# Performance work log

Measured on AMD Instinct MI355X. Metric: run time of the kernel, lower is better.

## Reference

```python
import jax, jax.numpy as jnp
import numpy as np

B, N, DIM = 4, 8192, 1024
HEADS, DIM_HEAD = 16, 64


def setup_inputs() -> dict:
    key = jax.random.key(0)
    ks = jax.random.split(key, 6)
    s = 1.0 / np.sqrt(DIM_HEAD)
    so = 1.0 / np.sqrt(HEADS * DIM_HEAD)
    return {
        "x": jax.random.normal(ks[0], (B, N, DIM), dtype=jnp.float32),
        "Wq": jax.random.uniform(ks[1], (DIM_HEAD, DIM_HEAD), jnp.float32, -s, s),
        "Wk": jax.random.uniform(ks[2], (DIM_HEAD, DIM_HEAD), jnp.float32, -s, s),
        "Wv": jax.random.uniform(ks[3], (DIM_HEAD, DIM_HEAD), jnp.float32, -s, s),
        "Wo": jax.random.uniform(ks[4], (DIM, HEADS * DIM_HEAD), jnp.float32, -so, so),
        "bo": jax.random.uniform(ks[5], (DIM,), jnp.float32, -so, so),
    }


def reference(x, Wq, Wk, Wv, Wo, bo):
    Bs, Ns, Cs = x.shape
    # [B, H, N, Dh]
    xh = x.reshape(Bs, Ns, HEADS, DIM_HEAD).transpose(0, 2, 1, 3)
    # torch Linear: y = x @ W.T
    q = jnp.einsum('bhnd,ed->bhne', xh, Wq)
    k = jnp.einsum('bhnd,ed->bhne', xh, Wk)
    v = jnp.einsum('bhnd,ed->bhne', xh, Wv)
    # k^T v: [B, H, Dh, Dh], normalized by N (dropout is identity, p=0)
    dots = jnp.einsum('bhnd,bhne->bhde', k, v) / float(Ns)
    res = jnp.einsum('bhnd,bhde->bhne', q, dots)
    # b h n d -> b n (h d)
    res = res.transpose(0, 2, 1, 3).reshape(Bs, Ns, HEADS * DIM_HEAD)
    return res @ Wo.T + bo
```

## Files before the change

### kernel.cpp

```cpp
#include <hip/hip_runtime.h>

#define DIMC 1024
#define NSEQ 8192
#define DH 64

typedef __attribute__((ext_vector_type(8))) short short8;
typedef __attribute__((ext_vector_type(4))) float f32x4;

__device__ __forceinline__ short f2bf(float f) {
  union { float f; unsigned u; } v; v.f = f;
  unsigned r = v.u + 0x7FFFu + ((v.u >> 16) & 1u);
  return (short)(r >> 16);
}

__device__ __forceinline__ void gload_lds16(const void* g, void* l) {
  __builtin_amdgcn_global_load_lds(
      (const __attribute__((address_space(1))) void*)g,
      (__attribute__((address_space(3))) void*)l, 16, 0, 0);
}

__global__ __launch_bounds__(64) void gram_kernel(const float* __restrict__ x,
                                                  float* __restrict__ Gpart) {
  int chunk = blockIdx.x, bh = blockIdx.y;
  int b = bh >> 4, h = bh & 15;
  int t = threadIdx.x;
  __shared__ __align__(16) float rows[16 * 64];
  const float* xb = x + ((size_t)b * NSEQ) * DIMC + h * DH;
  int d0 = (t >> 3) * 8, e0 = (t & 7) * 8;
  float acc[8][8] = {};
  for (int it = 0; it < 16; it++) {
    int nbase = chunk * 256 + it * 16;
    float4 v[4];
#pragma unroll
    for (int i = 0; i < 4; i++) {
      int f4 = i * 64 + t;
      v[i] = *(const float4*)(xb + (size_t)(nbase + (f4 >> 4)) * DIMC + (f4 & 15) * 4);
    }
    __syncthreads();
#pragma unroll
    for (int i = 0; i < 4; i++) ((float4*)rows)[i * 64 + t] = v[i];
    __syncthreads();
#pragma unroll
    for (int r = 0; r < 16; r++) {
      float xd[8], xe[8];
      *(float4*)&xd[0] = *(const float4*)&rows[r * 64 + d0];
      *(float4*)&xd[4] = *(const float4*)&rows[r * 64 + d0 + 4];
      *(float4*)&xe[0] = *(const float4*)&rows[r * 64 + e0];
      *(float4*)&xe[4] = *(const float4*)&rows[r * 64 + e0 + 4];
#pragma unroll
      for (int i = 0; i < 8; i++)
#pragma unroll
        for (int j = 0; j < 8; j++) acc[i][j] = fmaf(xd[i], xe[j], acc[i][j]);
    }
  }
  float* gp = Gpart + (size_t)chunk * (64 * 4096) + (size_t)bh * 4096;
#pragma unroll
  for (int i = 0; i < 8; i++)
#pragma unroll
    for (int j = 0; j < 8; j++) gp[(d0 + i) * 64 + e0 + j] = acc[i][j];
}

__global__ void reduce_g(const float* __restrict__ Gpart, float* __restrict__ G) {
  int i = blockIdx.x * 256 + threadIdx.x;
  float s = 0.f;
#pragma unroll
  for (int p = 0; p < 32; p++) s += Gpart[(size_t)p * (64 * 4096) + i];
  G[i] = s;
}

__global__ __launch_bounds__(256) void combine_kernel(
    const float* __restrict__ G, const float* __restrict__ Wq,
    const float* __restrict__ Wk, const float* __restrict__ Wv,
    const float* __restrict__ Wo, short* __restrict__ WbigT) {
  int bh = blockIdx.x, qt = blockIdx.y;
  int b = bh >> 4, h = bh & 15;
  int t = threadIdx.x;
  __shared__ __align__(16) float sG[4096];
  __shared__ __align__(16) float sW[4096];
  __shared__ __align__(16) float sA[4096];
  __shared__ __align__(16) float sM[4096];

  for (int i = t; i < 4096; i += 256) sG[i] = G[(size_t)bh * 4096 + i];
  for (int i = t; i < 4096; i += 256) sW[i] = Wk[i];
  __syncthreads();

  int d0 = (t >> 4) * 4, e0 = (t & 15) * 4;
  {
    float a[4][4] = {};
    for (int fg = 0; fg < 16; fg++) {
      float wk[4][4], g4[4][4];
#pragma unroll
      for (int i = 0; i < 4; i++) *(float4*)wk[i] = *(const float4*)&sW[(d0 + i) * 64 + fg * 4];
#pragma unroll
      for (int ff = 0; ff < 4; ff++) *(float4*)g4[ff] = *(const float4*)&sG[(fg * 4 + ff) * 64 + e0];
#pragma unroll
      for (int i = 0; i < 4; i++)
#pragma unroll
        for (int ff = 0; ff < 4; ff++)
#pragma unroll
          for (int j = 0; j < 4; j++) a[i][j] = fmaf(wk[i][ff], g4[ff][j], a[i][j]);
    }
#pragma unroll
    for (int i = 0; i < 4; i++)
#pragma unroll
      for (int j = 0; j < 4; j++) sA[(d0 + i) * 64 + e0 + j] = a[i][j];
  }
  __syncthreads();
  for (int i = t; i < 4096; i += 256) sW[i] = Wv[i];
  __syncthreads();
  {
    float a[4][4] = {};
    for (int fgi = 0; fgi < 16; fgi++) {
      int fg = (fgi + (t & 15)) & 15;
      float t1[4][4], wv[4][4];
#pragma unroll
      for (int i = 0; i < 4; i++) *(float4*)t1[i] = *(const float4*)&sA[(d0 + i) * 64 + fg * 4];
#pragma unroll
      for (int j = 0; j < 4; j++) *(float4*)wv[j] = *(const float4*)&sW[(e0 + j) * 64 + fg * 4];
#pragma unroll
      for (int i = 0; i < 4; i++)
#pragma unroll
        for (int j = 0; j < 4; j++)
#pragma unroll
          for (int ff = 0; ff < 4; ff++) a[i][j] = fmaf(t1[i][ff], wv[j][ff], a[i][j]);
    }
    __syncthreads();
#pragma unroll
    for (int i = 0; i < 4; i++)
#pragma unroll
      for (int j = 0; j < 4; j++) sG[(d0 + i) * 64 + e0 + j] = a[i][j];
  }
  __syncthreads();
  for (int i = t; i < 4096; i += 256) sW[i] = Wq[i];
  __syncthreads();
  {
    float a[4][4] = {};
    for (int f = 0; f < 64; f++) {
      float wq[4], t2[4];
      *(float4*)wq = *(const float4*)&sW[f * 64 + d0];
      *(float4*)t2 = *(const float4*)&sG[f * 64 + e0];
#pragma unroll
      for (int i = 0; i < 4; i++)
#pragma unroll
        for (int j = 0; j < 4; j++) a[i][j] = fmaf(wq[i], t2[j], a[i][j]);
    }
#pragma unroll
    for (int i = 0; i < 4; i++)
#pragma unroll
      for (int j = 0; j < 4; j++) sM[(d0 + i) * 64 + e0 + j] = a[i][j] * (1.0f / 8192.0f);
  }
  __syncthreads();
  int dd0 = (t & 15) * 4, cl0 = (t >> 4) * 4;
  for (int cc = qt * 4; cc < qt * 4 + 4; cc++) {
    int c0 = cc * 64;
    for (int i = t; i < 4096; i += 256)
      sW[i] = Wo[(size_t)(c0 + (i >> 6)) * DIMC + h * DH + (i & 63)];
    __syncthreads();
    float a[4][4] = {};
    for (int egi = 0; egi < 16; egi++) {
      int eg = (egi + (t & 15)) & 15;
      float m4[4][4], wo4[4][4];
#pragma unroll
      for (int i = 0; i < 4; i++) *(float4*)m4[i] = *(const float4*)&sM[(dd0 + i) * 64 + eg * 4];
#pragma unroll
      for (int j = 0; j < 4; j++) *(float4*)wo4[j] = *(const float4*)&sW[(cl0 + j) * 64 + eg * 4];
#pragma unroll
      for (int i = 0; i < 4; i++)
#pragma unroll
        for (int j = 0; j < 4; j++)
#pragma unroll
          for (int ff = 0; ff < 4; ff++) a[i][j] = fmaf(m4[i][ff], wo4[j][ff], a[i][j]);
    }
#pragma unroll
    for (int j = 0; j < 4; j++)
#pragma unroll
      for (int i = 0; i < 4; i++)
        WbigT[((size_t)b << 20) + (size_t)(c0 + cl0 + j) * DIMC + h * DH + dd0 + i] =
            f2bf(a[i][j]);
    __syncthreads();
  }
}

__global__ __launch_bounds__(256, 2) void gemm_kernel(
    const float* __restrict__ x, const short* __restrict__ WbigT,
    const float* __restrict__ bo, float* __restrict__ out) {
  int bid = blockIdx.x;
  int xcd = bid & 7, r = bid >> 3;
  int g = r >> 5, q = r & 31;
  int m_blk = g * 32 + xcd * 4 + (q >> 3);
  int n_blk = q & 7;
  int b = m_blk >> 6;
  int row0 = m_blk * 128;
  int c0 = n_blk * 128;

  __shared__ __align__(16) short As[128 * 32];
  __shared__ __align__(16) short Bs[128 * 32];

  int t = threadIdx.x;
  int lane = t & 63, wave = t >> 6;
  int wm = wave >> 1, wn = wave & 1;
  int quad = lane >> 4, ln = lane & 15;

  f32x4 acc[4][4];
#pragma unroll
  for (int i = 0; i < 4; i++)
#pragma unroll
    for (int j = 0; j < 4; j++) acc[i][j] = (f32x4){0.f, 0.f, 0.f, 0.f};

  const short* Bbase = WbigT + ((size_t)b << 20);

  for (int kt = 0; kt < 32; kt++) {
    int k0 = kt * 32;
    __syncthreads();
#pragma unroll
    for (int L = 0; L < 2; L++) {
      int elem = (wave * 2 + L) * 512 + lane * 8;
      int crow = elem >> 5, koff = elem & 31;
      gload_lds16(Bbase + (size_t)(c0 + crow) * DIMC + k0 + koff, &Bs[elem]);
    }
#pragma unroll
    for (int qq = 0; qq < 2; qq++) {
      int elem = qq * 2048 + wave * 512 + lane * 8;
      int m = elem >> 5, kk = elem & 31;
      const float* gp = x + (size_t)(row0 + m) * DIMC + k0 + kk;
      float4 v0 = *(const float4*)gp;
      float4 v1 = *(const float4*)(gp + 4);
      short8 pk;
      pk[0] = f2bf(v0.x); pk[1] = f2bf(v0.y); pk[2] = f2bf(v0.z); pk[3] = f2bf(v0.w);
      pk[4] = f2bf(v1.x); pk[5] = f2bf(v1.y); pk[6] = f2bf(v1.z); pk[7] = f2bf(v1.w);
      *(short8*)&As[elem] = pk;
    }
    __syncthreads();
    short8 afrag[4], bfrag[4];
#pragma unroll
    for (int i = 0; i < 4; i++) {
      afrag[i] = *(const short8*)&As[(wm * 64 + i * 16 + ln) * 32 + quad * 8];
      bfrag[i] = *(const short8*)&Bs[(wn * 64 + i * 16 + ln) * 32 + quad * 8];
    }
#pragma unroll
    for (int i = 0; i < 4; i++)
#pragma unroll
      for (int j = 0; j < 4; j++)
        acc[i][j] = __builtin_amdgcn_mfma_f32_16x16x32_bf16(afrag[i], bfrag[j], acc[i][j], 0, 0, 0);
  }

  float bov[4];
#pragma unroll
  for (int j = 0; j < 4; j++) bov[j] = bo[c0 + wn * 64 + j * 16 + ln];
#pragma unroll
  for (int i = 0; i < 4; i++)
#pragma unroll
    for (int j = 0; j < 4; j++) {
      int col = c0 + wn * 64 + j * 16 + ln;
#pragma unroll
      for (int rr = 0; rr < 4; rr++) {
        int row = row0 + wm * 64 + i * 16 + quad * 4 + rr;
        out[(size_t)row * DIMC + col] = acc[i][j][rr] + bov[j];
      }
    }
}

extern "C" void kernel_launch(void* const* d_in, const int* in_sizes, int n_in,
                              void* d_out, int out_size, void* d_ws, size_t ws_size,
                              hipStream_t stream) {
  const float* x  = (const float*)d_in[0];
  const float* Wq = (const float*)d_in[1];
  const float* Wk = (const float*)d_in[2];
  const float* Wv = (const float*)d_in[3];
  const float* Wo = (const float*)d_in[4];
  const float* bo = (const float*)d_in[5];
  float* out = (float*)d_out;

  float* Gpart = (float*)d_ws;
  float* G     = (float*)((char*)d_ws + ((size_t)32 << 20));
  short* WbigT = (short*)((char*)d_ws + ((size_t)33 << 20));
  (void)in_sizes; (void)n_in; (void)out_size; (void)ws_size;

  gram_kernel<<<dim3(32, 64), 64, 0, stream>>>(x, Gpart);
  reduce_g<<<1024, 256, 0, stream>>>(Gpart, G);
  combine_kernel<<<dim3(64, 4), 256, 0, stream>>>(G, Wq, Wk, Wv, Wo, WbigT);
  gemm_kernel<<<2048, 256, 0, stream>>>(x, WbigT, bo, out);
}
```

Measured before the change: 434.4 us.

## Software-pipeline gram and GEMM loads, double-buffer B with swizzled LDS

In the gram kernel, the next 16-row tile is now prefetched into registers while the current tile is being computed. In the GEMM, B tiles are double-buffered in LDS with an XOR swizzle meant to avoid bank conflicts. A is now loaded from global memory straight into MFMA fragments in registers, with the next tile prefetched during the current MFMAs, which drops the A LDS buffer and one barrier per iteration. It also uses a cheaper bf16 conversion with round-half-up instead of round-to-nearest-even, and asks for 3 blocks per CU in exchange for more register pressure.

```diff
diff --git a/kernel.cpp b/kernel.cpp
--- a/kernel.cpp
+++ b/kernel.cpp
@@ -11,6 +11,14 @@
   union { float f; unsigned u; } v; v.f = f;
   unsigned r = v.u + 0x7FFFu + ((v.u >> 16) & 1u);
   return (short)(r >> 16);
+}
+
+__device__ __forceinline__ unsigned pack_bf2(float a, float b) {
+  union { float f; unsigned u; } va, vb;
+  va.f = a; vb.f = b;
+  unsigned ua = va.u + 0x8000u;
+  unsigned ub = vb.u + 0x8000u;
+  return (ua >> 16) | (ub & 0xFFFF0000u);
 }
 
 __device__ __forceinline__ void gload_lds16(const void* g, void* l) {
@@ -28,18 +36,25 @@
   const float* xb = x + ((size_t)b * NSEQ) * DIMC + h * DH;
   int d0 = (t >> 3) * 8, e0 = (t & 7) * 8;
   float acc[8][8] = {};
+  float4 v[4];
+#pragma unroll
+  for (int i = 0; i < 4; i++) {
+    int f4 = i * 64 + t;
+    v[i] = *(const float4*)(xb + (size_t)(chunk * 256 + (f4 >> 4)) * DIMC + (f4 & 15) * 4);
+  }
   for (int it = 0; it < 16; it++) {
-    int nbase = chunk * 256 + it * 16;
-    float4 v[4];
-#pragma unroll
-    for (int i = 0; i < 4; i++) {
-      int f4 = i * 64 + t;
-      v[i] = *(const float4*)(xb + (size_t)(nbase + (f4 >> 4)) * DIMC + (f4 & 15) * 4);
-    }
     __syncthreads();
 #pragma unroll
     for (int i = 0; i < 4; i++) ((float4*)rows)[i * 64 + t] = v[i];
     __syncthreads();
+    if (it < 15) {
+      int nbase = chunk * 256 + (it + 1) * 16;
+#pragma unroll
+      for (int i = 0; i < 4; i++) {
+        int f4 = i * 64 + t;
+        v[i] = *(const float4*)(xb + (size_t)(nbase + (f4 >> 4)) * DIMC + (f4 & 15) * 4);
+      }
+    }
 #pragma unroll
     for (int r = 0; r < 16; r++) {
       float xd[8], xe[8];
@@ -181,7 +196,7 @@
   }
 }
 
-__global__ __launch_bounds__(256, 2) void gemm_kernel(
+__global__ __launch_bounds__(256, 3) void gemm_kernel(
     const float* __restrict__ x, const short* __restrict__ WbigT,
     const float* __restrict__ bo, float* __restrict__ out) {
   int bid = blockIdx.x;
@@ -193,8 +208,7 @@
   int row0 = m_blk * 128;
   int c0 = n_blk * 128;
 
-  __shared__ __align__(16) short As[128 * 32];
-  __shared__ __align__(16) short Bs[128 * 32];
+  __shared__ __align__(16) short Bs[2][128 * 32];
 
   int t = threadIdx.x;
   int lane = t & 63, wave = t >> 6;
@@ -208,40 +222,76 @@
     for (int j = 0; j < 4; j++) acc[i][j] = (f32x4){0.f, 0.f, 0.f, 0.f};
 
   const short* Bbase = WbigT + ((size_t)b << 20);
+  const float* Abase = x + (size_t)(row0 + wm * 64 + ln) * DIMC + quad * 8;
+
+  int e_base[2], crow_[2], lc_[2];
+#pragma unroll
+  for (int L = 0; L < 2; L++) {
+    int e = (wave * 2 + L) * 512 + lane * 8;
+    e_base[L] = e;
+    int crow = e >> 5;
+    int p = (e >> 3) & 3;
+    crow_[L] = crow;
+    lc_[L] = p ^ ((crow >> 1) & 3);
+  }
+
+#define STAGE_B(KT, BUF)                                                        \
+  {                                                                             \
+    int k0s = (KT) * 32;                                                        \
+    _Pragma("unroll") for (int L = 0; L < 2; L++) {                             \
+      gload_lds16(Bbase + (size_t)(c0 + crow_[L]) * DIMC + k0s + lc_[L] * 8,    \
+                  &Bs[BUF][e_base[L]]);                                         \
+    }                                                                           \
+  }
+
+#define LOAD_A_RAW(KT, DST)                                                     \
+  {                                                                             \
+    int k0s = (KT) * 32;                                                        \
+    _Pragma("unroll") for (int i = 0; i < 4; i++) {                             \
+      const float* gp = Abase + (size_t)i * 16 * DIMC + k0s;                    \
+      DST[i][0] = *(const float4*)gp;                                           \
+      DST[i][1] = *(const float4*)(gp + 4);                                     \
+    }                                                                           \
+  }
+
+#define CVT_A(SRC, AF)                                                          \
+  {                                                                             \
+    _Pragma("unroll") for (int i = 0; i < 4; i++) {                             \
+      unsigned w0 = pack_bf2(SRC[i][0].x, SRC[i][0].y);                         \
+      unsigned w1 = pack_bf2(SRC[i][0].z, SRC[i][0].w);                         \
+      unsigned w2 = pack_bf2(SRC[i][1].x, SRC[i][1].y);                         \
+      unsigned w3 = pack_bf2(SRC[i][1].z, SRC[i][1].w);                         \
+      unsigned tmp[4] = {w0, w1, w2, w3};                                       \
+      AF[i] = *(short8*)tmp;                                                    \
+    }                                                                           \
+  }
+
+  float4 araw[4][2];
+  short8 afrag[4];
+  STAGE_B(0, 0);
+  LOAD_A_RAW(0, araw);
+  CVT_A(araw, afrag);
 
   for (int kt = 0; kt < 32; kt++) {
-    int k0 = kt * 32;
-    __syncthreads();
-#pragma unroll
-    for (int L = 0; L < 2; L++) {
-      int elem = (wave * 2 + L) * 512 + lane * 8;
-      int crow = elem >> 5, koff = elem & 31;
-      gload_lds16(Bbase + (size_t)(c0 + crow) * DIMC + k0 + koff, &Bs[elem]);
-    }
-#pragma unroll
-    for (int qq = 0; qq < 2; qq++) {
-      int elem = qq * 2048 + wave * 512 + lane * 8;
-      int m = elem >> 5, kk = elem & 31;
-      const float* gp = x + (size_t)(row0 + m) * DIMC + k0 + kk;
-      float4 v0 = *(const float4*)gp;
-      float4 v1 = *(const float4*)(gp + 4);
-      short8 pk;
-      pk[0] = f2bf(v0.x); pk[1] = f2bf(v0.y); pk[2] = f2bf(v0.z); pk[3] = f2bf(v0.w);
-      pk[4] = f2bf(v1.x); pk[5] = f2bf(v1.y); pk[6] = f2bf(v1.z); pk[7] = f2bf(v1.w);
-      *(short8*)&As[elem] = pk;
-    }
-    __syncthreads();
-    short8 afrag[4], bfrag[4];
+    __syncthreads();
+    if (kt < 31) {
+      STAGE_B(kt + 1, (kt + 1) & 1);
+      LOAD_A_RAW(kt + 1, araw);
+    }
+    const short* bs = Bs[kt & 1];
+    short8 bfrag[4];
 #pragma unroll
     for (int i = 0; i < 4; i++) {
-      afrag[i] = *(const short8*)&As[(wm * 64 + i * 16 + ln) * 32 + quad * 8];
-      bfrag[i] = *(const short8*)&Bs[(wn * 64 + i * 16 + ln) * 32 + quad * 8];
+      int brow = wn * 64 + i * 16 + ln;
+      int pc = quad ^ ((brow >> 1) & 3);
+      bfrag[i] = *(const short8*)&bs[brow * 32 + pc * 8];
     }
 #pragma unroll
     for (int i = 0; i < 4; i++)
 #pragma unroll
       for (int j = 0; j < 4; j++)
         acc[i][j] = __builtin_amdgcn_mfma_f32_16x16x32_bf16(afrag[i], bfrag[j], acc[i][j], 0, 0, 0);
+    if (kt < 31) CVT_A(araw, afrag);
   }
 
   float bov[4];
@@ -258,6 +308,9 @@
         out[(size_t)row * DIMC + col] = acc[i][j][rr] + bov[j];
       }
     }
+#undef STAGE_B
+#undef LOAD_A_RAW
+#undef CVT_A
 }
 
 extern "C" void kernel_launch(void* const* d_in, const int* in_sizes, int n_in,
```

Result: slower. 575.6 us (+32.5%).

## Emit bf16 copy of x in gram pass and feed GEMM via direct LDS loads

Applied to the files above, without the earlier changes.

The gram kernel now also writes a bf16 copy of x (when workspace allows) and software-prefetches the next row tile. The main GEMM then loads both operands straight into LDS with global_load_lds, so it reads half the bytes and skips per-tile conversion. LDS tiles get an XOR swizzle to cut bank conflicts, combine work is spread over twice as many blocks, and occupancy is raised to 3 blocks per SM. Rounding changes to round-half-up, the extra xbf write adds traffic, and the path depends on workspace size.

```diff
diff --git a/kernel.cpp b/kernel.cpp
--- a/kernel.cpp
+++ b/kernel.cpp
@@ -13,6 +13,14 @@
   return (short)(r >> 16);
 }
 
+__device__ __forceinline__ unsigned pack_bf2(float a, float b) {
+  union { float f; unsigned u; } va, vb;
+  va.f = a; vb.f = b;
+  unsigned ua = va.u + 0x8000u;
+  unsigned ub = vb.u + 0x8000u;
+  return (ua >> 16) | (ub & 0xFFFF0000u);
+}
+
 __device__ __forceinline__ void gload_lds16(const void* g, void* l) {
   __builtin_amdgcn_global_load_lds(
       (const __attribute__((address_space(1))) void*)g,
@@ -20,26 +28,44 @@
 }
 
 __global__ __launch_bounds__(64) void gram_kernel(const float* __restrict__ x,
-                                                  float* __restrict__ Gpart) {
+                                                  float* __restrict__ Gpart,
+                                                  short* __restrict__ xbf) {
   int chunk = blockIdx.x, bh = blockIdx.y;
   int b = bh >> 4, h = bh & 15;
   int t = threadIdx.x;
   __shared__ __align__(16) float rows[16 * 64];
   const float* xb = x + ((size_t)b * NSEQ) * DIMC + h * DH;
+  short* xo = xbf ? xbf + ((size_t)b * NSEQ) * DIMC + h * DH : (short*)0;
   int d0 = (t >> 3) * 8, e0 = (t & 7) * 8;
   float acc[8][8] = {};
+  float4 v[4];
+#pragma unroll
+  for (int i = 0; i < 4; i++) {
+    int f4 = i * 64 + t;
+    v[i] = *(const float4*)(xb + (size_t)(chunk * 256 + (f4 >> 4)) * DIMC + (f4 & 15) * 4);
+  }
   for (int it = 0; it < 16; it++) {
-    int nbase = chunk * 256 + it * 16;
-    float4 v[4];
-#pragma unroll
-    for (int i = 0; i < 4; i++) {
-      int f4 = i * 64 + t;
-      v[i] = *(const float4*)(xb + (size_t)(nbase + (f4 >> 4)) * DIMC + (f4 & 15) * 4);
-    }
     __syncthreads();
 #pragma unroll
     for (int i = 0; i < 4; i++) ((float4*)rows)[i * 64 + t] = v[i];
     __syncthreads();
+    if (xo) {
+#pragma unroll
+      for (int i = 0; i < 4; i++) {
+        int f4 = i * 64 + t;
+        int row = chunk * 256 + it * 16 + (f4 >> 4), col = (f4 & 15) * 4;
+        uint2 pw = {pack_bf2(v[i].x, v[i].y), pack_bf2(v[i].z, v[i].w)};
+        *(uint2*)(xo + (size_t)row * DIMC + col) = pw;
+      }
+    }
+    if (it < 15) {
+      int nbase = chunk * 256 + (it + 1) * 16;
+#pragma unroll
+      for (int i = 0; i < 4; i++) {
+        int f4 = i * 64 + t;
+        v[i] = *(const float4*)(xb + (size_t)(nbase + (f4 >> 4)) * DIMC + (f4 & 15) * 4);
+      }
+    }
 #pragma unroll
     for (int r = 0; r < 16; r++) {
       float xd[8], xe[8];
@@ -151,7 +177,7 @@
   }
   __syncthreads();
   int dd0 = (t & 15) * 4, cl0 = (t >> 4) * 4;
-  for (int cc = qt * 4; cc < qt * 4 + 4; cc++) {
+  for (int cc = qt * 2; cc < qt * 2 + 2; cc++) {
     int c0 = cc * 64;
     for (int i = t; i < 4096; i += 256)
       sW[i] = Wo[(size_t)(c0 + (i >> 6)) * DIMC + h * DH + (i & 63)];
@@ -172,16 +198,15 @@
           for (int ff = 0; ff < 4; ff++) a[i][j] = fmaf(m4[i][ff], wo4[j][ff], a[i][j]);
     }
 #pragma unroll
-    for (int j = 0; j < 4; j++)
-#pragma unroll
-      for (int i = 0; i < 4; i++)
-        WbigT[((size_t)b << 20) + (size_t)(c0 + cl0 + j) * DIMC + h * DH + dd0 + i] =
-            f2bf(a[i][j]);
-    __syncthreads();
-  }
-}
-
-__global__ __launch_bounds__(256, 2) void gemm_kernel(
+    for (int j = 0; j < 4; j++) {
+      uint2 pw = {pack_bf2(a[0][j], a[1][j]), pack_bf2(a[2][j], a[3][j])};
+      *(uint2*)&WbigT[((size_t)b << 20) + (size_t)(c0 + cl0 + j) * DIMC + h * DH + dd0] = pw;
+    }
+    __syncthreads();
+  }
+}
+
+__global__ __launch_bounds__(256, 3) void gemm_small(
     const float* __restrict__ x, const short* __restrict__ WbigT,
     const float* __restrict__ bo, float* __restrict__ out) {
   int bid = blockIdx.x;
@@ -209,15 +234,22 @@
 
   const short* Bbase = WbigT + ((size_t)b << 20);
 
+  int e_base[2], crow_[2], lc_[2];
+#pragma unroll
+  for (int L = 0; L < 2; L++) {
+    int e = (wave * 2 + L) * 512 + lane * 8;
+    e_base[L] = e;
+    int crow = e >> 5;
+    crow_[L] = crow;
+    lc_[L] = ((e >> 3) & 3) ^ ((crow >> 1) & 3);
+  }
+
   for (int kt = 0; kt < 32; kt++) {
     int k0 = kt * 32;
     __syncthreads();
 #pragma unroll
-    for (int L = 0; L < 2; L++) {
-      int elem = (wave * 2 + L) * 512 + lane * 8;
-      int crow = elem >> 5, koff = elem & 31;
-      gload_lds16(Bbase + (size_t)(c0 + crow) * DIMC + k0 + koff, &Bs[elem]);
-    }
+    for (int L = 0; L < 2; L++)
+      gload_lds16(Bbase + (size_t)(c0 + crow_[L]) * DIMC + k0 + lc_[L] * 8, &Bs[e_base[L]]);
 #pragma unroll
     for (int qq = 0; qq < 2; qq++) {
       int elem = qq * 2048 + wave * 512 + lane * 8;
@@ -225,17 +257,100 @@
       const float* gp = x + (size_t)(row0 + m) * DIMC + k0 + kk;
       float4 v0 = *(const float4*)gp;
       float4 v1 = *(const float4*)(gp + 4);
-      short8 pk;
-      pk[0] = f2bf(v0.x); pk[1] = f2bf(v0.y); pk[2] = f2bf(v0.z); pk[3] = f2bf(v0.w);
-      pk[4] = f2bf(v1.x); pk[5] = f2bf(v1.y); pk[6] = f2bf(v1.z); pk[7] = f2bf(v1.w);
-      *(short8*)&As[elem] = pk;
+      unsigned w0 = pack_bf2(v0.x, v0.y), w1 = pack_bf2(v0.z, v0.w);
+      unsigned w2 = pack_bf2(v1.x, v1.y), w3 = pack_bf2(v1.z, v1.w);
+      unsigned tmp[4] = {w0, w1, w2, w3};
+      int pe = ((elem >> 3) & 3) ^ ((m >> 1) & 3);
+      *(short8*)&As[m * 32 + pe * 8] = *(short8*)tmp;
     }
     __syncthreads();
     short8 afrag[4], bfrag[4];
 #pragma unroll
     for (int i = 0; i < 4; i++) {
-      afrag[i] = *(const short8*)&As[(wm * 64 + i * 16 + ln) * 32 + quad * 8];
-      bfrag[i] = *(const short8*)&Bs[(wn * 64 + i * 16 + ln) * 32 + quad * 8];
+      int ar = wm * 64 + i * 16 + ln;
+      afrag[i] = *(const short8*)&As[ar * 32 + (quad ^ ((ar >> 1) & 3)) * 8];
+      int br = wn * 64 + i * 16 + ln;
+      bfrag[i] = *(const short8*)&Bs[br * 32 + (quad ^ ((br >> 1) & 3)) * 8];
+    }
+#pragma unroll
+    for (int i = 0; i < 4; i++)
+#pragma unroll
+      for (int j = 0; j < 4; j++)
+        acc[i][j] = __builtin_amdgcn_mfma_f32_16x16x32_bf16(afrag[i], bfrag[j], acc[i][j], 0, 0, 0);
+  }
+
+  float bov[4];
+#pragma unroll
+  for (int j = 0; j < 4; j++) bov[j] = bo[c0 + wn * 64 + j * 16 + ln];
+#pragma unroll
+  for (int i = 0; i < 4; i++)
+#pragma unroll
+    for (int j = 0; j < 4; j++) {
+      int col = c0 + wn * 64 + j * 16 + ln;
+#pragma unroll
+      for (int rr = 0; rr < 4; rr++) {
+        int row = row0 + wm * 64 + i * 16 + quad * 4 + rr;
+        out[(size_t)row * DIMC + col] = acc[i][j][rr] + bov[j];
+      }
+    }
+}
+
+__global__ __launch_bounds__(256, 3) void gemm_big(
+    const short* __restrict__ xbf, const short* __restrict__ WbigT,
+    const float* __restrict__ bo, float* __restrict__ out) {
+  int bid = blockIdx.x;
+  int xcd = bid & 7, r = bid >> 3;
+  int g = r >> 5, q = r & 31;
+  int m_blk = g * 32 + xcd * 4 + (q >> 3);
+  int n_blk = q & 7;
+  int b = m_blk >> 6;
+  int row0 = m_blk * 128;
+  int c0 = n_blk * 128;
+
+  __shared__ __align__(16) short As[128 * 32];
+  __shared__ __align__(16) short Bs[128 * 32];
+
+  int t = threadIdx.x;
+  int lane = t & 63, wave = t >> 6;
+  int wm = wave >> 1, wn = wave & 1;
+  int quad = lane >> 4, ln = lane & 15;
+
+  f32x4 acc[4][4];
+#pragma unroll
+  for (int i = 0; i < 4; i++)
+#pragma unroll
+    for (int j = 0; j < 4; j++) acc[i][j] = (f32x4){0.f, 0.f, 0.f, 0.f};
+
+  const short* Bbase = WbigT + ((size_t)b << 20);
+
+  int e_base[2];
+  const short* Asrc[2];
+  const short* Bsrc[2];
+#pragma unroll
+  for (int L = 0; L < 2; L++) {
+    int e = (wave * 2 + L) * 512 + lane * 8;
+    e_base[L] = e;
+    int row = e >> 5;
+    int lc = ((e >> 3) & 3) ^ ((row >> 1) & 3);
+    Asrc[L] = xbf + (size_t)(row0 + row) * DIMC + lc * 8;
+    Bsrc[L] = Bbase + (size_t)(c0 + row) * DIMC + lc * 8;
+  }
+
+  for (int kt = 0; kt < 32; kt++) {
+    int k0 = kt * 32;
+    __syncthreads();
+#pragma unroll
+    for (int L = 0; L < 2; L++) gload_lds16(Asrc[L] + k0, &As[e_base[L]]);
+#pragma unroll
+    for (int L = 0; L < 2; L++) gload_lds16(Bsrc[L] + k0, &Bs[e_base[L]]);
+    __syncthreads();
+    short8 afrag[4], bfrag[4];
+#pragma unroll
+    for (int i = 0; i < 4; i++) {
+      int ar = wm * 64 + i * 16 + ln;
+      afrag[i] = *(const short8*)&As[ar * 32 + (quad ^ ((ar >> 1) & 3)) * 8];
+      int br = wn * 64 + i * 16 + ln;
+      bfrag[i] = *(const short8*)&Bs[br * 32 + (quad ^ ((br >> 1) & 3)) * 8];
     }
 #pragma unroll
     for (int i = 0; i < 4; i++)
@@ -270,14 +385,24 @@
   const float* Wo = (const float*)d_in[4];
   const float* bo = (const float*)d_in[5];
   float* out = (float*)d_out;
-
-  float* Gpart = (float*)d_ws;
-  float* G     = (float*)((char*)d_ws + ((size_t)32 << 20));
-  short* WbigT = (short*)((char*)d_ws + ((size_t)33 << 20));
-  (void)in_sizes; (void)n_in; (void)out_size; (void)ws_size;
-
-  gram_kernel<<<dim3(32, 64), 64, 0, stream>>>(x, Gpart);
-  reduce_g<<<1024, 256, 0, stream>>>(Gpart, G);
-  combine_kernel<<<dim3(64, 4), 256, 0, stream>>>(G, Wq, Wk, Wv, Wo, WbigT);
-  gemm_kernel<<<2048, 256, 0, stream>>>(x, WbigT, bo, out);
-}
+  (void)in_sizes; (void)n_in; (void)out_size;
+
+  if (ws_size >= ((size_t)105 << 20)) {
+    short* xbf   = (short*)d_ws;
+    float* Gpart = (float*)((char*)d_ws + ((size_t)64 << 20));
+    float* G     = (float*)((char*)d_ws + ((size_t)96 << 20));
+    short* WbigT = (short*)((char*)d_ws + ((size_t)97 << 20));
+    gram_kernel<<<dim3(32, 64), 64, 0, stream>>>(x, Gpart, xbf);
+    reduce_g<<<1024, 256, 0, stream>>>(Gpart, G);
+    combine_kernel<<<dim3(64, 8), 256, 0, stream>>>(G, Wq, Wk, Wv, Wo, WbigT);
+    gemm_big<<<2048, 256, 0, stream>>>(xbf, WbigT, bo, out);
+  } else {
+    float* Gpart = (float*)d_ws;
+    float* G     = (float*)((char*)d_ws + ((size_t)32 << 20));
+    short* WbigT = (short*)((char*)d_ws + ((size_t)33 << 20));
+    gram_kernel<<<dim3(32, 64), 64, 0, stream>>>(x, Gpart, (short*)0);
+    reduce_g<<<1024, 256, 0, stream>>>(Gpart, G);
+    combine_kernel<<<dim3(64, 8), 256, 0, stream>>>(G, Wq, Wk, Wv, Wo, WbigT);
+    gemm_small<<<2048, 256, 0, stream>>>(x, WbigT, bo, out);
+  }
+}
```

Result: faster. 378.6 us (-12.8%).
